# Kernel optimization log

Measured on AMD Instinct MI355X. Metric: run time of the kernel, lower is better.

Reference implementation:

```python
import jax, jax.numpy as jnp
import numpy as np

N_SP, N_SPAT = 20000, 10000
E_SS, E_BIP, E_SP = 160000, 320000, 320000
H, C = 4, 64  # GAT heads / per-head channels (hidden_channels=64, concat=False)
EPS = 1e-6


def _gat(xs, xd, row, col, ea, Ws, Wd, a_s, a_d, a_e, We, b, num_dst, heads, ch, self_loops, concat):
    # PyG GATConv with edge_dim: linear -> per-head additive attention -> softmax over incoming edges -> scatter-add
    hs = (xs @ Ws).reshape(-1, heads, ch)          # [Ns,H,C]
    hd = (xd @ Wd).reshape(-1, heads, ch)          # [Nd,H,C]
    al_s = jnp.sum(hs * a_s, -1)                   # [Ns,H]
    al_d = jnp.sum(hd * a_d, -1)                   # [Nd,H]
    if self_loops:
        # add_self_loops with fill_value='mean': loop edge_attr = mean of incoming edge_attr per node
        cnt = jax.ops.segment_sum(jnp.ones((row.shape[0],), ea.dtype), col, num_dst)
        loop_ea = jax.ops.segment_sum(ea, col, num_dst) / jnp.maximum(cnt, 1.0)[:, None]
        loops = jnp.arange(num_dst, dtype=row.dtype)
        row = jnp.concatenate([row, loops])
        col = jnp.concatenate([col, loops])
        ea = jnp.concatenate([ea, loop_ea], 0)
    he = (ea @ We).reshape(-1, heads, ch)          # [E,H,C]
    al = jax.nn.leaky_relu(al_s[row] + al_d[col] + jnp.sum(he * a_e, -1), 0.2)  # [E,H]
    m = jax.ops.segment_max(al, col, num_segments=num_dst)
    ex = jnp.exp(al - m[col])
    den = jax.ops.segment_sum(ex, col, num_segments=num_dst)
    alpha = ex / (den[col] + 1e-16)
    out = jax.ops.segment_sum(hs[row] * alpha[..., None], col, num_segments=num_dst)  # [Nd,H,C]
    out = out.reshape(num_dst, heads * ch) if concat else out.mean(1)
    return out + b


def setup_inputs() -> dict:
    key = jax.random.key(0)
    ks = iter(jax.random.split(key, 64))
    f = lambda shape: jax.random.normal(next(ks), shape, jnp.float32)
    w = lambda shape: f(shape) / np.sqrt(shape[0])
    inp = {}
    inp['species_x_mean'] = f((N_SP, 32))
    inp['species_x_std'] = jax.random.uniform(next(ks), (N_SP, 32), jnp.float32)
    inp['traits_nanmask'] = jax.random.bernoulli(next(ks), 0.4, (N_SP, 32))
    inp['species_x_gen'] = f((N_SP, 64))
    inp['species_x_phylo'] = f((N_SP, 128))
    inp['spatial_x'] = f((N_SPAT, 12))
    inp['spatial_global_data'] = f((N_SPAT, 4))
    ei = lambda e, ns, nd: jnp.stack([jax.random.randint(next(ks), (e,), 0, ns, jnp.int32),
                                      jax.random.randint(next(ks), (e,), 0, nd, jnp.int32)])
    inp['ss_edge_index'] = ei(E_SS, N_SPAT, N_SPAT)
    inp['ss_edge_attr'] = jax.random.uniform(next(ks), (E_SS, 1), jnp.float32)
    inp['bip_edge_index'] = ei(E_BIP, N_SPAT, N_SP)
    inp['bip_edge_attr'] = jax.random.uniform(next(ks), (E_BIP, 1), jnp.float32)
    inp['sp_edge_index'] = ei(E_SP, N_SP, N_SP)
    inp['sp_edge_attr'] = jax.random.uniform(next(ks), (E_SP, 1), jnp.float32)
    # GAT conv params: space_gnn (sg0, sg1), species_gnn (pg0, pg1)
    for nm, din in [('sg0', 16), ('sg1', 64), ('pg0', 128), ('pg1', 64)]:
        inp[nm + '_W'] = w((din, H * C))
        inp[nm + '_as'] = f((H, C)) * 0.1
        inp[nm + '_ad'] = f((H, C)) * 0.1
        inp[nm + '_ae'] = f((H, C)) * 0.1
        inp[nm + '_We'] = w((1, H * C))
        inp[nm + '_b'] = jnp.zeros((C,), jnp.float32)
    # bipartite GATConv: heads=1, concat=True, src dim=hidden=64, dst dim=in_gen+in_phylo=192
    inp['bp_Ws'] = w((64, 64))
    inp['bp_Wd'] = w((192, 64))
    inp['bp_as'] = f((1, 64)) * 0.1
    inp['bp_ad'] = f((1, 64)) * 0.1
    inp['bp_ae'] = f((1, 64)) * 0.1
    inp['bp_We'] = w((1, 64))
    inp['bp_b'] = jnp.zeros((64,), jnp.float32)
    inp['sl_W'] = w((288, 64))
    inp['sl_b'] = jnp.zeros((64,), jnp.float32)
    inp['fc_W'] = w((64, 64))
    inp['fc_b'] = jnp.zeros((64,), jnp.float32)
    return inp


def reference(species_x_mean, species_x_std, traits_nanmask, species_x_gen, species_x_phylo,
              spatial_x, spatial_global_data, ss_edge_index, ss_edge_attr, bip_edge_index,
              bip_edge_attr, sp_edge_index, sp_edge_attr,
              sg0_W, sg0_as, sg0_ad, sg0_ae, sg0_We, sg0_b,
              sg1_W, sg1_as, sg1_ad, sg1_ae, sg1_We, sg1_b,
              pg0_W, pg0_as, pg0_ad, pg0_ae, pg0_We, pg0_b,
              pg1_W, pg1_as, pg1_ad, pg1_ae, pg1_We, pg1_b,
              bp_Ws, bp_Wd, bp_as, bp_ad, bp_ae, bp_We, bp_b,
              sl_W, sl_b, fc_W, fc_b):
    # inference path: no trait masking -> visibility = observed mask
    vis = (~traits_nanmask).astype(jnp.float32)
    sp_in = jnp.concatenate([species_x_mean, species_x_std, vis, species_x_gen, species_x_phylo], 1)
    sp_in = jax.nn.relu(sp_in @ sl_W + sl_b)                      # [N_SP,64]
    # spatial GNN (2 GATConv layers, heads=4, concat=False, self loops)
    h = jnp.concatenate([spatial_x, spatial_global_data], 1)      # [N_SPAT,16]
    r, c = ss_edge_index[0], ss_edge_index[1]
    h = jax.nn.relu(_gat(h, h, r, c, ss_edge_attr, sg0_W, sg0_W, sg0_as, sg0_ad, sg0_ae, sg0_We, sg0_b, N_SPAT, H, C, True, False))
    h = jax.nn.relu(_gat(h, h, r, c, ss_edge_attr, sg1_W, sg1_W, sg1_as, sg1_ad, sg1_ae, sg1_We, sg1_b, N_SPAT, H, C, True, False))
    # bipartite spatial->species GATConv (heads=1, concat=True, no self loops)
    part = jnp.concatenate([species_x_gen, species_x_phylo], 1)   # [N_SP,192]
    br, bc = bip_edge_index[0], bip_edge_index[1]
    sts = jax.nn.relu(_gat(h, part, br, bc, bip_edge_attr, bp_Ws, bp_Wd, bp_as, bp_ad, bp_ae, bp_We, bp_b, N_SP, 1, 64, False, True))
    # species GNN (2 GATConv layers)
    x = jnp.concatenate([sts, sp_in], 1)                          # [N_SP,128]
    pr, pc = sp_edge_index[0], sp_edge_index[1]
    x = jax.nn.relu(_gat(x, x, pr, pc, sp_edge_attr, pg0_W, pg0_W, pg0_as, pg0_ad, pg0_ae, pg0_We, pg0_b, N_SP, H, C, True, False))
    x = jax.nn.relu(_gat(x, x, pr, pc, sp_edge_attr, pg1_W, pg1_W, pg1_as, pg1_ad, pg1_ae, pg1_We, pg1_b, N_SP, H, C, True, False))
    ms = x @ fc_W + fc_b                                          # [N_SP, 2*out]
    mean, log_std = jnp.split(ms, 2, axis=-1)
    std = jax.nn.softplus(log_std) + EPS
    return mean, std
```

## Files before the change

kernel.cpp:

```cpp
#include <hip/hip_runtime.h>
#include <hip/hip_bf16.h>

#define NSP   20000
#define NSPAT 10000
#define ESS   160000
#define EBIP  320000
#define ESP   320000

static inline int cdiv_host(long a, long b) { return (int)((a + b - 1) / b); }

__device__ __forceinline__ float wave_red_sum(float p) {
#pragma unroll
  for (int m = 32; m >= 1; m >>= 1) p += __shfl_xor(p, m, 64);
  return p;
}

__device__ __forceinline__ float bf2f(unsigned short u) {
  return __uint_as_float(((unsigned int)u) << 16);
}
__device__ __forceinline__ unsigned short f2bf(float f) {
  unsigned int u = __float_as_uint(f);
  unsigned int r = (u + 0x7FFF + ((u >> 16) & 1)) >> 16;
  return (unsigned short)r;
}

__global__ void build_pre_kernel(const float* __restrict__ mean, const float* __restrict__ stdv,
                                 const void* __restrict__ mask, const int* __restrict__ flag,
                                 const float* __restrict__ sx, const float* __restrict__ sg,
                                 float* __restrict__ spc96, float* __restrict__ h0) {
  const long totA = (long)NSP * 96;
  const long totB = (long)NSPAT * 16;
  int mode = *flag;
  for (long i = (long)blockIdx.x * blockDim.x + threadIdx.x; i < totA + totB;
       i += (long)gridDim.x * blockDim.x) {
    if (i < totA) {
      int n = (int)(i / 96), c = (int)(i % 96);
      float v;
      if (c < 32) v = mean[(long)n * 32 + c];
      else if (c < 64) v = stdv[(long)n * 32 + (c - 32)];
      else {
        long j = (long)n * 32 + (c - 64);
        int mv;
        if (mode == 0) mv = ((const int*)mask)[j];
        else if (mode == 2) mv = (((const float*)mask)[j] != 0.0f);
        else mv = (int)((const unsigned char*)mask)[j];
        v = mv ? 0.f : 1.f;
      }
      spc96[i] = v;
    } else {
      long k = i - totA;
      int n = (int)(k / 16), c = (int)(k % 16);
      h0[k] = (c < 12) ? sx[(long)n * 12 + c] : sg[(long)n * 4 + (c - 12)];
    }
  }
}

__global__ void count3_kernel(
    const int* c1, int E1, int* cp1, int* rnk1, int n1,
    const int* c2, int E2, int* cp2, int* rnk2, int n2,
    const int* c3, int E3, int* cp3, int* rnk3, int n3) {
  int total = E1 + E2 + E3;
  for (int i = blockIdx.x * blockDim.x + threadIdx.x; i < total; i += gridDim.x * blockDim.x) {
    int p = (i >> 8) & 7;
    if (i < E1) {
      int d = c1[i]; rnk1[i] = atomicAdd(&cp1[p * n1 + d], 1);
    } else if (i < E1 + E2) {
      int j = i - E1;
      int d = c2[j]; rnk2[j] = atomicAdd(&cp2[p * n2 + d], 1);
    } else {
      int j = i - E1 - E2;
      int d = c3[j]; rnk3[j] = atomicAdd(&cp3[p * n3 + d], 1);
    }
  }
}

__global__ void merge3_kernel(int* cp1, int* c1, int n1,
                              int* cp2, int* c2, int n2,
                              int* cp3, int* c3, int n3) {
  int i = blockIdx.x * blockDim.x + threadIdx.x;
  int total = n1 + n2 + n3;
  if (i >= total) return;
  int *cp, *c; int n, d;
  if (i < n1) { cp = cp1; c = c1; n = n1; d = i; }
  else if (i < n1 + n2) { cp = cp2; c = c2; n = n2; d = i - n1; }
  else { cp = cp3; c = c3; n = n3; d = i - n1 - n2; }
  int s = 0;
#pragma unroll
  for (int p = 0; p < 8; ++p) { int t = cp[p * n + d]; cp[p * n + d] = s; s += t; }
  c[d] = s;
}

__global__ __launch_bounds__(1024) void scan3_kernel(
    const int* cntA, int nA, int* ptrA,
    const int* cntB, int nB, int* ptrB,
    const int* cntC, int nC, int* ptrC) {
  const int* cnt; int n; int* ptr;
  if (blockIdx.x == 0) { cnt = cntA; n = nA; ptr = ptrA; }
  else if (blockIdx.x == 1) { cnt = cntB; n = nB; ptr = ptrB; }
  else { cnt = cntC; n = nC; ptr = ptrC; }
  __shared__ int part[1024];
  int t = threadIdx.x;
  int ch = (n + 1023) / 1024;
  int beg = t * ch, end = min(beg + ch, n);
  int s = 0;
  for (int i = beg; i < end; ++i) s += cnt[i];
  part[t] = s;
  __syncthreads();
  for (int off = 1; off < 1024; off <<= 1) {
    int v = (t >= off) ? part[t - off] : 0;
    __syncthreads();
    part[t] += v;
    __syncthreads();
  }
  int run = (t == 0) ? 0 : part[t - 1];
  for (int i = beg; i < end; ++i) { ptr[i] = run; run += cnt[i]; }
  if (t == 1023) ptr[n] = part[1023];
}

__global__ void scatter3_kernel(
    const int* r1, const int* c1, const float* e1, int E1, const int* p1, const int* cp1, const int* k1, int n1, int* s1, float* a1,
    const int* r2, const int* c2, const float* e2, int E2, const int* p2, const int* cp2, const int* k2, int n2, int* s2, float* a2,
    const int* r3, const int* c3, const float* e3, int E3, const int* p3, const int* cp3, const int* k3, int n3, int* s3, float* a3) {
  int total = E1 + E2 + E3;
  for (int i = blockIdx.x * blockDim.x + threadIdx.x; i < total; i += gridDim.x * blockDim.x) {
    int p = (i >> 8) & 7;
    if (i < E1) {
      int d = c1[i];
      int pos = p1[d] + cp1[p * n1 + d] + k1[i];
      s1[pos] = r1[i]; a1[pos] = e1[i];
    } else if (i < E1 + E2) {
      int j = i - E1;
      int d = c2[j];
      int pos = p2[d] + cp2[p * n2 + d] + k2[j];
      s2[pos] = r2[j]; a2[pos] = e2[j];
    } else {
      int j = i - E1 - E2;
      int d = c3[j];
      int pos = p3[d] + cp3[p * n3 + d] + k3[j];
      s3[pos] = r3[j]; a3[pos] = e3[j];
    }
  }
}

__global__ void leafin_csr2(const int* ptrA, const float* ceaA, int nA, float* leaA,
                            const int* ptrB, const float* ceaB, int nB, float* leaB) {
  int i = blockIdx.x * blockDim.x + threadIdx.x;
  if (i >= nA + nB) return;
  const int* ptr; const float* cea; float* lea; int d;
  if (i < nA) { ptr = ptrA; cea = ceaA; lea = leaA; d = i; }
  else { ptr = ptrB; cea = ceaB; lea = leaB; d = i - nA; }
  int e0 = ptr[d], e1 = ptr[d + 1];
  float s = 0.f;
  for (int e = e0; e < e1; ++e) s += cea[e];
  lea[d] = s / (float)max(e1 - e0, 1);
}

__global__ void dote_all_kernel(const float* __restrict__ We0, const float* __restrict__ ae0,
                                const float* __restrict__ We1, const float* __restrict__ ae1,
                                const float* __restrict__ Web, const float* __restrict__ aeb,
                                const float* __restrict__ We2, const float* __restrict__ ae2,
                                const float* __restrict__ We3, const float* __restrict__ ae3,
                                const unsigned int* __restrict__ mask,
                                float* __restrict__ dotes, int* __restrict__ flag) {
  int b = blockIdx.x, t = threadIdx.x;
  if (b == 5) {
    if (t < 64) {
      unsigned int w0 = mask[t], w1 = mask[t + 64], w2 = mask[t + 128], w3 = mask[t + 192];
      bool ai = (w0 <= 1u) && (w1 <= 1u) && (w2 <= 1u) && (w3 <= 1u);
      auto okf = [](unsigned int w) { return w == 0u || w == 0x3f800000u; };
      bool af = okf(w0) && okf(w1) && okf(w2) && okf(w3);
      unsigned long long bi = __ballot(ai), bf = __ballot(af);
      if (t == 0) *flag = (bi == ~0ull) ? 0 : ((bf == ~0ull) ? 2 : 1);
    }
    return;
  }
  const float *We, *ae;
  int n, off;
  switch (b) {
    case 0: We = We0; ae = ae0; n = 256; off = 0; break;
    case 1: We = We1; ae = ae1; n = 256; off = 4; break;
    case 2: We = Web; ae = aeb; n = 64;  off = 8; break;
    case 3: We = We2; ae = ae2; n = 256; off = 12; break;
    default: We = We3; ae = ae3; n = 256; off = 16; break;
  }
  if (t < n) {
    float p = wave_red_sum(We[t] * ae[t]);
    if ((t & 63) == 0) dotes[off + (t >> 6)] = p;
  }
}

struct XSrc { const float* p[5]; int w[5]; int n; };

__global__ __launch_bounds__(256) void proj64_kernel(
    XSrc xsrc, int M, int K,
    const float* __restrict__ W, const float* __restrict__ bias, int mode,
    const float* __restrict__ a_s, const float* __restrict__ a_d,
    float* __restrict__ al_s, float* __restrict__ al_d,
    float* __restrict__ Y, float* __restrict__ Y2) {
  constexpr int KC = 32;
  constexpr int BR = 32;
  constexpr int KCP = 36;
  __shared__ float wl[KC * 64];
  __shared__ float xl[BR * KCP];

  int t = threadIdx.x;
  int cg = t & 15, rg = t >> 4;
  int c0 = cg * 4;
  long row0 = (long)blockIdx.x * BR;

  float acc[2][4];
#pragma unroll
  for (int r = 0; r < 2; ++r)
#pragma unroll
    for (int j = 0; j < 4; ++j) acc[r][j] = 0.f;

  for (int k0 = 0; k0 < K; k0 += KC) {
    int seg = 0; int base = 0;
    while (k0 >= base + xsrc.w[seg]) { base += xsrc.w[seg]; ++seg; }
    const float* Xp = xsrc.p[seg];
    int stride = xsrc.w[seg];
    int kloc = k0 - base;

    __syncthreads();
    {
      const float4* ws = (const float4*)(W + (long)k0 * 64);
      float4* wd = (float4*)wl;
      wd[t] = ws[t];
      wd[t + 256] = ws[t + 256];
    }
    {
      int r = t >> 3, kq = (t & 7) * 4;
      long rr = row0 + r; if (rr >= M) rr = M - 1;
      float4 v = *(const float4*)(Xp + rr * stride + kloc + kq);
      *(float4*)(xl + r * KCP + kq) = v;
    }
    __syncthreads();

    for (int kg = 0; kg < KC; kg += 4) {
      float4 w0 = *(const float4*)(wl + (kg + 0) * 64 + c0);
      float4 w1 = *(const float4*)(wl + (kg + 1) * 64 + c0);
      float4 w2 = *(const float4*)(wl + (kg + 2) * 64 + c0);
      float4 w3 = *(const float4*)(wl + (kg + 3) * 64 + c0);
#pragma unroll
      for (int r = 0; r < 2; ++r) {
        float4 xv = *(const float4*)(xl + (rg * 2 + r) * KCP + kg);
        acc[r][0] = fmaf(xv.x, w0.x, acc[r][0]);
        acc[r][1] = fmaf(xv.x, w0.y, acc[r][1]);
        acc[r][2] = fmaf(xv.x, w0.z, acc[r][2]);
        acc[r][3] = fmaf(xv.x, w0.w, acc[r][3]);
        acc[r][0] = fmaf(xv.y, w1.x, acc[r][0]);
        acc[r][1] = fmaf(xv.y, w1.y, acc[r][1]);
        acc[r][2] = fmaf(xv.y, w1.z, acc[r][2]);
        acc[r][3] = fmaf(xv.y, w1.w, acc[r][3]);
        acc[r][0] = fmaf(xv.z, w2.x, acc[r][0]);
        acc[r][1] = fmaf(xv.z, w2.y, acc[r][1]);
        acc[r][2] = fmaf(xv.z, w2.z, acc[r][2]);
        acc[r][3] = fmaf(xv.z, w2.w, acc[r][3]);
        acc[r][0] = fmaf(xv.w, w3.x, acc[r][0]);
        acc[r][1] = fmaf(xv.w, w3.y, acc[r][1]);
        acc[r][2] = fmaf(xv.w, w3.z, acc[r][2]);
        acc[r][3] = fmaf(xv.w, w3.w, acc[r][3]);
      }
    }
  }

  float4 bv = make_float4(0.f, 0.f, 0.f, 0.f);
  float4 asv = make_float4(0.f, 0.f, 0.f, 0.f);
  float4 adv = make_float4(0.f, 0.f, 0.f, 0.f);
  if (bias) bv = *(const float4*)(bias + c0);
  if (a_s) asv = *(const float4*)(a_s + c0);
  if (a_d) adv = *(const float4*)(a_d + c0);

#pragma unroll
  for (int r = 0; r < 2; ++r) {
    long m = row0 + rg * 2 + r;
    bool ok = m < M;
    float v0 = acc[r][0] + bv.x, v1 = acc[r][1] + bv.y;
    float v2 = acc[r][2] + bv.z, v3 = acc[r][3] + bv.w;
    if (mode == 1) {
      if (ok)
        *(float4*)(Y + m * 64 + c0) = make_float4(
            fmaxf(v0, 0.f), fmaxf(v1, 0.f), fmaxf(v2, 0.f), fmaxf(v3, 0.f));
    } else if (mode == 2) {
      if (ok) {
        if (c0 < 32) {
          *(float4*)(Y + m * 32 + c0) = make_float4(v0, v1, v2, v3);
        } else {
          float4 o;
          o.x = fmaxf(v0, 0.f) + log1pf(__expf(-fabsf(v0))) + 1e-6f;
          o.y = fmaxf(v1, 0.f) + log1pf(__expf(-fabsf(v1))) + 1e-6f;
          o.z = fmaxf(v2, 0.f) + log1pf(__expf(-fabsf(v2))) + 1e-6f;
          o.w = fmaxf(v3, 0.f) + log1pf(__expf(-fabsf(v3))) + 1e-6f;
          *(float4*)(Y2 + m * 32 + (c0 - 32)) = o;
        }
      }
    } else if (ok && Y) {
      *(float4*)(Y + m * 64 + c0) = make_float4(v0, v1, v2, v3);
    }
    if (a_s) {
      float s = acc[r][0] * asv.x + acc[r][1] * asv.y + acc[r][2] * asv.z + acc[r][3] * asv.w;
      s += __shfl_xor(s, 1); s += __shfl_xor(s, 2);
      s += __shfl_xor(s, 4); s += __shfl_xor(s, 8);
      if (ok && cg == 0) al_s[m] = s;
    }
    if (a_d) {
      float s = acc[r][0] * adv.x + acc[r][1] * adv.y + acc[r][2] * adv.z + acc[r][3] * adv.w;
      s += __shfl_xor(s, 1); s += __shfl_xor(s, 2);
      s += __shfl_xor(s, 4); s += __shfl_xor(s, 8);
      if (ok && cg == 0) al_d[m] = s;
    }
  }
}

__global__ __launch_bounds__(256) void proj_kernel(
    XSrc xsrc, int M, int K,
    const float* __restrict__ W, const float* __restrict__ bias, int mode,
    const float* __restrict__ a_s, const float* __restrict__ a_d,
    float* __restrict__ al_s, float* __restrict__ al_d,
    float* __restrict__ Y, float* __restrict__ Y2) {
  constexpr int NOUT = 256;
  constexpr int KC = 32;
  constexpr int RPT = 8;
  constexpr int BR = 32;
  constexpr int KCP = 36;
  constexpr int H = 4;
  __shared__ float wl[KC * NOUT];
  __shared__ float xl[BR * KCP];

  int t = threadIdx.x;
  int cg = t & 63, rg = t >> 6;
  int c0 = cg * 4;
  long row0 = (long)blockIdx.x * BR;

  float acc[RPT][4];
#pragma unroll
  for (int r = 0; r < RPT; ++r)
#pragma unroll
    for (int j = 0; j < 4; ++j) acc[r][j] = 0.f;

  for (int k0 = 0; k0 < K; k0 += KC) {
    int kc = min(KC, K - k0);
    int seg = 0; int base = 0;
    while (k0 >= base + xsrc.w[seg]) { base += xsrc.w[seg]; ++seg; }
    const float* Xp = xsrc.p[seg];
    int stride = xsrc.w[seg];
    int kloc = k0 - base;

    __syncthreads();
    {
      const float4* wsrc = (const float4*)(W + (long)k0 * NOUT);
      float4* wdst = (float4*)wl;
      for (int i = t; i < (kc * NOUT) >> 2; i += 256) wdst[i] = wsrc[i];
    }
    for (int i = t; i < BR * 8; i += 256) {
      int r = i >> 3, kq = (i & 7) * 4;
      if (kq < kc) {
        long rr = row0 + r; if (rr >= M) rr = M - 1;
        float4 v = *(const float4*)(Xp + rr * stride + kloc + kq);
        *(float4*)(xl + r * KCP + kq) = v;
      }
    }
    __syncthreads();

    for (int kg = 0; kg < kc; kg += 4) {
      float4 w0 = *(const float4*)(wl + (kg + 0) * NOUT + c0);
      float4 w1 = *(const float4*)(wl + (kg + 1) * NOUT + c0);
      float4 w2 = *(const float4*)(wl + (kg + 2) * NOUT + c0);
      float4 w3 = *(const float4*)(wl + (kg + 3) * NOUT + c0);
      float4 xv[RPT];
#pragma unroll
      for (int r = 0; r < RPT; ++r)
        xv[r] = *(const float4*)(xl + (rg * RPT + r) * KCP + kg);
#pragma unroll
      for (int r = 0; r < RPT; ++r) {
        acc[r][0] = fmaf(xv[r].x, w0.x, acc[r][0]);
        acc[r][1] = fmaf(xv[r].x, w0.y, acc[r][1]);
        acc[r][2] = fmaf(xv[r].x, w0.z, acc[r][2]);
        acc[r][3] = fmaf(xv[r].x, w0.w, acc[r][3]);
        acc[r][0] = fmaf(xv[r].y, w1.x, acc[r][0]);
        acc[r][1] = fmaf(xv[r].y, w1.y, acc[r][1]);
        acc[r][2] = fmaf(xv[r].y, w1.z, acc[r][2]);
        acc[r][3] = fmaf(xv[r].y, w1.w, acc[r][3]);
        acc[r][0] = fmaf(xv[r].z, w2.x, acc[r][0]);
        acc[r][1] = fmaf(xv[r].z, w2.y, acc[r][1]);
        acc[r][2] = fmaf(xv[r].z, w2.z, acc[r][2]);
        acc[r][3] = fmaf(xv[r].z, w2.w, acc[r][3]);
        acc[r][0] = fmaf(xv[r].w, w3.x, acc[r][0]);
        acc[r][1] = fmaf(xv[r].w, w3.y, acc[r][1]);
        acc[r][2] = fmaf(xv[r].w, w3.z, acc[r][2]);
        acc[r][3] = fmaf(xv[r].w, w3.w, acc[r][3]);
      }
    }
  }

  float4 asv = make_float4(0.f, 0.f, 0.f, 0.f);
  float4 adv = make_float4(0.f, 0.f, 0.f, 0.f);
  if (a_s) asv = *(const float4*)(a_s + c0);
  if (a_d) adv = *(const float4*)(a_d + c0);

#pragma unroll
  for (int r = 0; r < RPT; ++r) {
    long m = row0 + (long)rg * RPT + r;
    bool ok = m < M;
    if (ok && mode == 3) {
      ushort4 o;
      o.x = f2bf(acc[r][0]); o.y = f2bf(acc[r][1]);
      o.z = f2bf(acc[r][2]); o.w = f2bf(acc[r][3]);
      *(ushort4*)((unsigned short*)Y + m * NOUT + c0) = o;
    }
    if (a_s) {
      float s = acc[r][0] * asv.x + acc[r][1] * asv.y + acc[r][2] * asv.z + acc[r][3] * asv.w;
      s += __shfl_xor(s, 1); s += __shfl_xor(s, 2);
      s += __shfl_xor(s, 4); s += __shfl_xor(s, 8);
      if (ok && (cg & 15) == 0) al_s[m * H + (c0 >> 6)] = s;
    }
    if (a_d) {
      float s = acc[r][0] * adv.x + acc[r][1] * adv.y + acc[r][2] * adv.z + acc[r][3] * adv.w;
      s += __shfl_xor(s, 1); s += __shfl_xor(s, 2);
      s += __shfl_xor(s, 4); s += __shfl_xor(s, 8);
      if (ok && (cg & 15) == 0) al_d[m * H + (c0 >> 6)] = s;
    }
  }
  (void)bias; (void)Y2;
}

__device__ __forceinline__ void fma4_bf(float4& a, float al, ushort4 u) {
  a.x = fmaf(al, bf2f(u.x), a.x); a.y = fmaf(al, bf2f(u.y), a.y);
  a.z = fmaf(al, bf2f(u.z), a.z); a.w = fmaf(al, bf2f(u.w), a.w);
}
__device__ __forceinline__ void scale4(float4& a, float s) {
  a.x *= s; a.y *= s; a.z *= s; a.w *= s;
}

template <bool SELFLOOP>
__global__ __launch_bounds__(256) void gat4_fused(
    int Nd, const int* __restrict__ dptr, const int* __restrict__ csr_src,
    const float* __restrict__ csr_ea, const float* __restrict__ al_s,
    const float* __restrict__ al_d, const float* __restrict__ dote,
    const float* __restrict__ loop_ea, const unsigned short* __restrict__ hs,
    const float* __restrict__ bias, float* __restrict__ out) {
  int wave = threadIdx.x >> 6, lane = threadIdx.x & 63;
  int n = blockIdx.x * 4 + wave;
  if (n >= Nd) return;
  int h = lane >> 4;
  float ald = al_d[(long)n * 4 + h];
  float de = dote[h];
  int e0 = dptr[n], e1 = dptr[n + 1];
  float m0 = -INFINITY, d0 = 0.f;
  float4 a0 = make_float4(0.f, 0.f, 0.f, 0.f);
  if (SELFLOOP) {
    float l = al_s[(long)n * 4 + h] + ald + loop_ea[n] * de;
    l = (l > 0.f) ? l : 0.2f * l;
    m0 = l; d0 = 1.f;
    ushort4 u = *(const ushort4*)(hs + (long)n * 256 + lane * 4);
    a0.x = bf2f(u.x); a0.y = bf2f(u.y); a0.z = bf2f(u.z); a0.w = bf2f(u.w);
  }
  float m1 = -INFINITY, d1 = 0.f;
  float4 a1 = make_float4(0.f, 0.f, 0.f, 0.f);
  int e = e0;
  for (; e + 2 <= e1; e += 2) {
    int s0 = csr_src[e], s1 = csr_src[e + 1];
    float l0 = al_s[(long)s0 * 4 + h] + ald + csr_ea[e] * de;
    float l1 = al_s[(long)s1 * 4 + h] + ald + csr_ea[e + 1] * de;
    l0 = (l0 > 0.f) ? l0 : 0.2f * l0;
    l1 = (l1 > 0.f) ? l1 : 0.2f * l1;
    ushort4 u0 = *(const ushort4*)(hs + (long)s0 * 256 + lane * 4);
    ushort4 u1 = *(const ushort4*)(hs + (long)s1 * 256 + lane * 4);
    if (l0 > m0) { float sc = __expf(m0 - l0); d0 *= sc; scale4(a0, sc); m0 = l0; }
    float ex0 = __expf(l0 - m0);
    d0 += ex0;
    fma4_bf(a0, ex0, u0);
    if (l1 > m1) { float sc = __expf(m1 - l1); d1 *= sc; scale4(a1, sc); m1 = l1; }
    float ex1 = __expf(l1 - m1);
    d1 += ex1;
    fma4_bf(a1, ex1, u1);
  }
  if (e < e1) {
    int s0 = csr_src[e];
    float l0 = al_s[(long)s0 * 4 + h] + ald + csr_ea[e] * de;
    l0 = (l0 > 0.f) ? l0 : 0.2f * l0;
    ushort4 u0 = *(const ushort4*)(hs + (long)s0 * 256 + lane * 4);
    if (l0 > m0) { float sc = __expf(m0 - l0); d0 *= sc; scale4(a0, sc); m0 = l0; }
    float ex0 = __expf(l0 - m0);
    d0 += ex0;
    fma4_bf(a0, ex0, u0);
  }
  if (m1 != -INFINITY) {
    float M = fmaxf(m0, m1);
    float sA = (m0 == -INFINITY) ? 0.f : __expf(m0 - M);
    float sB = __expf(m1 - M);
    d0 = d0 * sA + d1 * sB;
    a0.x = a0.x * sA + a1.x * sB; a0.y = a0.y * sA + a1.y * sB;
    a0.z = a0.z * sA + a1.z * sB; a0.w = a0.w * sA + a1.w * sB;
  }
  float inv = 1.f / (d0 + 1e-16f);
  scale4(a0, inv);
  a0.x += __shfl_xor(a0.x, 16); a0.y += __shfl_xor(a0.y, 16);
  a0.z += __shfl_xor(a0.z, 16); a0.w += __shfl_xor(a0.w, 16);
  a0.x += __shfl_xor(a0.x, 32); a0.y += __shfl_xor(a0.y, 32);
  a0.z += __shfl_xor(a0.z, 32); a0.w += __shfl_xor(a0.w, 32);
  if (lane < 16) {
    float4 b = *(const float4*)(bias + lane * 4);
    float4 o;
    o.x = fmaxf(a0.x * 0.25f + b.x, 0.f);
    o.y = fmaxf(a0.y * 0.25f + b.y, 0.f);
    o.z = fmaxf(a0.z * 0.25f + b.z, 0.f);
    o.w = fmaxf(a0.w * 0.25f + b.w, 0.f);
    *(float4*)(out + (long)n * 64 + lane * 4) = o;
  }
}

__global__ __launch_bounds__(256) void gat1_fused(
    int Nd, const int* __restrict__ dptr, const int* __restrict__ csr_src,
    const float* __restrict__ csr_ea, const float* __restrict__ al_s,
    const float* __restrict__ al_d, const float* __restrict__ dote,
    const float* __restrict__ hs, const float* __restrict__ bias,
    float* __restrict__ out) {
  int wave = threadIdx.x >> 6, lane = threadIdx.x & 63;
  int n = blockIdx.x * 4 + wave;
  if (n >= Nd) return;
  float ald = al_d[n];
  float de = dote[0];
  int e0 = dptr[n], e1 = dptr[n + 1];
  float m0 = -INFINITY, d0 = 0.f, acc0 = 0.f;
  float m1 = -INFINITY, d1 = 0.f, acc1 = 0.f;
  int e = e0;
  for (; e + 2 <= e1; e += 2) {
    int s0 = csr_src[e], s1 = csr_src[e + 1];
    float l0 = al_s[s0] + ald + csr_ea[e] * de;
    float l1 = al_s[s1] + ald + csr_ea[e + 1] * de;
    l0 = (l0 > 0.f) ? l0 : 0.2f * l0;
    l1 = (l1 > 0.f) ? l1 : 0.2f * l1;
    float h0 = hs[(long)s0 * 64 + lane];
    float h1 = hs[(long)s1 * 64 + lane];
    if (l0 > m0) { float sc = __expf(m0 - l0); d0 *= sc; acc0 *= sc; m0 = l0; }
    float ex0 = __expf(l0 - m0);
    d0 += ex0; acc0 = fmaf(ex0, h0, acc0);
    if (l1 > m1) { float sc = __expf(m1 - l1); d1 *= sc; acc1 *= sc; m1 = l1; }
    float ex1 = __expf(l1 - m1);
    d1 += ex1; acc1 = fmaf(ex1, h1, acc1);
  }
  if (e < e1) {
    int s0 = csr_src[e];
    float l0 = al_s[s0] + ald + csr_ea[e] * de;
    l0 = (l0 > 0.f) ? l0 : 0.2f * l0;
    float h0 = hs[(long)s0 * 64 + lane];
    if (l0 > m0) { float sc = __expf(m0 - l0); d0 *= sc; acc0 *= sc; m0 = l0; }
    float ex0 = __expf(l0 - m0);
    d0 += ex0; acc0 = fmaf(ex0, h0, acc0);
  }
  if (m1 != -INFINITY) {
    float M = fmaxf(m0, m1);
    float sA = (m0 == -INFINITY) ? 0.f : __expf(m0 - M);
    float sB = __expf(m1 - M);
    d0 = d0 * sA + d1 * sB;
    acc0 = acc0 * sA + acc1 * sB;
  }
  float o = acc0 / (d0 + 1e-16f);
  out[(long)n * 64 + lane] = fmaxf(o + bias[lane], 0.f);
}

extern "C" void kernel_launch(void* const* d_in, const int* in_sizes, int n_in,
                              void* d_out, int out_size, void* d_ws, size_t ws_size,
                              hipStream_t stream) {
  const float* sp_mean = (const float*)d_in[0];
  const float* sp_std  = (const float*)d_in[1];
  const void*  nanmask = d_in[2];
  const float* sp_gen  = (const float*)d_in[3];
  const float* sp_phy  = (const float*)d_in[4];
  const float* spat_x  = (const float*)d_in[5];
  const float* spat_g  = (const float*)d_in[6];
  const int*   ss_ei   = (const int*)d_in[7];
  const float* ss_ea   = (const float*)d_in[8];
  const int*   bip_ei  = (const int*)d_in[9];
  const float* bip_ea  = (const float*)d_in[10];
  const int*   sp_ei   = (const int*)d_in[11];
  const float* sp_ea   = (const float*)d_in[12];
  const float* sg0_W = (const float*)d_in[13]; const float* sg0_as = (const float*)d_in[14];
  const float* sg0_ad = (const float*)d_in[15]; const float* sg0_ae = (const float*)d_in[16];
  const float* sg0_We = (const float*)d_in[17]; const float* sg0_b = (const float*)d_in[18];
  const float* sg1_W = (const float*)d_in[19]; const float* sg1_as = (const float*)d_in[20];
  const float* sg1_ad = (const float*)d_in[21]; const float* sg1_ae = (const float*)d_in[22];
  const float* sg1_We = (const float*)d_in[23]; const float* sg1_b = (const float*)d_in[24];
  const float* pg0_W = (const float*)d_in[25]; const float* pg0_as = (const float*)d_in[26];
  const float* pg0_ad = (const float*)d_in[27]; const float* pg0_ae = (const float*)d_in[28];
  const float* pg0_We = (const float*)d_in[29]; const float* pg0_b = (const float*)d_in[30];
  const float* pg1_W = (const float*)d_in[31]; const float* pg1_as = (const float*)d_in[32];
  const float* pg1_ad = (const float*)d_in[33]; const float* pg1_ae = (const float*)d_in[34];
  const float* pg1_We = (const float*)d_in[35]; const float* pg1_b = (const float*)d_in[36];
  const float* bp_Ws = (const float*)d_in[37]; const float* bp_Wd = (const float*)d_in[38];
  const float* bp_as = (const float*)d_in[39]; const float* bp_ad = (const float*)d_in[40];
  const float* bp_ae = (const float*)d_in[41]; const float* bp_We = (const float*)d_in[42];
  const float* bp_b  = (const float*)d_in[43];
  const float* sl_W  = (const float*)d_in[44]; const float* sl_b  = (const float*)d_in[45];
  const float* fc_W  = (const float*)d_in[46]; const float* fc_b  = (const float*)d_in[47];

  char* wsb = (char*)d_ws;
  size_t off = 0;
  auto A = [&](size_t nbytes) -> void* {
    void* p = wsb + off;
    off += (nbytes + 255) & ~(size_t)255;
    return p;
  };
  int* ss_cp = (int*)A((size_t)8 * NSPAT * 4);
  int* bp_cp = (int*)A((size_t)8 * NSP * 4);
  int* pp_cp = (int*)A((size_t)8 * NSP * 4);
  size_t zbytes = off;
  int*   ss_cnt = (int*)A((NSPAT + 1) * 4);
  int*   bp_cnt = (int*)A((NSP + 1) * 4);
  int*   pp_cnt = (int*)A((NSP + 1) * 4);
  int*   flag  = (int*)A(4);
  float* dotes = (float*)A(5 * 4 * sizeof(float));
  float* alS   = (float*)A((size_t)NSP * 4 * 4);
  float* alD   = (float*)A((size_t)NSP * 4 * 4);
  float* spc96 = (float*)A((size_t)NSP * 96 * 4);
  float* sp_in = (float*)A((size_t)NSP * 64 * 4);
  float* h0    = (float*)A((size_t)NSPAT * 16 * 4);
  float* h_a   = (float*)A((size_t)NSPAT * 64 * 4);
  float* h_b   = (float*)A((size_t)NSPAT * 64 * 4);
  float* HS    = (float*)A((size_t)NSP * 256 * 4);
  float* sts   = (float*)A((size_t)NSP * 64 * 4);
  float* x1    = (float*)A((size_t)NSP * 64 * 4);
  int*   ss_ptr = (int*)A((NSPAT + 1) * 4);
  int*   ss_src = (int*)A((size_t)ESS * 4);
  float* ss_cea = (float*)A((size_t)ESS * 4);
  int*   ss_rnk = (int*)A((size_t)ESS * 4);
  float* ss_lea = (float*)A((size_t)NSPAT * 4);
  int*   bp_ptr = (int*)A((NSP + 1) * 4);
  int*   bp_src = (int*)A((size_t)EBIP * 4);
  float* bp_cea = (float*)A((size_t)EBIP * 4);
  int*   bp_rnk = (int*)A((size_t)EBIP * 4);
  int*   pp_ptr = (int*)A((NSP + 1) * 4);
  int*   pp_src = (int*)A((size_t)ESP * 4);
  float* pp_cea = (float*)A((size_t)ESP * 4);
  int*   pp_rnk = (int*)A((size_t)ESP * 4);
  float* pp_lea = (float*)A((size_t)NSP * 4);
  (void)ws_size; (void)in_sizes; (void)n_in; (void)out_size;

  const int TB = 256;
  hipMemsetAsync(wsb, 0, zbytes, stream);

  count3_kernel<<<cdiv_host(ESS + EBIP + ESP, TB), TB, 0, stream>>>(
      ss_ei + ESS, ESS, ss_cp, ss_rnk, NSPAT,
      bip_ei + EBIP, EBIP, bp_cp, bp_rnk, NSP,
      sp_ei + ESP, ESP, pp_cp, pp_rnk, NSP);
  merge3_kernel<<<cdiv_host(NSPAT + NSP + NSP, TB), TB, 0, stream>>>(
      ss_cp, ss_cnt, NSPAT, bp_cp, bp_cnt, NSP, pp_cp, pp_cnt, NSP);
  scan3_kernel<<<3, 1024, 0, stream>>>(ss_cnt, NSPAT, ss_ptr, bp_cnt, NSP, bp_ptr, pp_cnt, NSP, pp_ptr);
  scatter3_kernel<<<cdiv_host(ESS + EBIP + ESP, TB), TB, 0, stream>>>(
      ss_ei, ss_ei + ESS, ss_ea, ESS, ss_ptr, ss_cp, ss_rnk, NSPAT, ss_src, ss_cea,
      bip_ei, bip_ei + EBIP, bip_ea, EBIP, bp_ptr, bp_cp, bp_rnk, NSP, bp_src, bp_cea,
      sp_ei, sp_ei + ESP, sp_ea, ESP, pp_ptr, pp_cp, pp_rnk, NSP, pp_src, pp_cea);
  leafin_csr2<<<cdiv_host(NSPAT + NSP, TB), TB, 0, stream>>>(
      ss_ptr, ss_cea, NSPAT, ss_lea, pp_ptr, pp_cea, NSP, pp_lea);

  dote_all_kernel<<<6, 256, 0, stream>>>(sg0_We, sg0_ae, sg1_We, sg1_ae, bp_We, bp_ae,
                                         pg0_We, pg0_ae, pg1_We, pg1_ae,
                                         (const unsigned int*)nanmask, dotes, flag);

  build_pre_kernel<<<cdiv_host((long)NSP * 96 + (long)NSPAT * 16, TB), TB, 0, stream>>>(
      sp_mean, sp_std, nanmask, flag, spat_x, spat_g, spc96, h0);

  {
    XSrc xs{}; xs.p[0] = spc96; xs.w[0] = 96; xs.p[1] = sp_gen; xs.w[1] = 64;
    xs.p[2] = sp_phy; xs.w[2] = 128; xs.n = 3;
    proj64_kernel<<<cdiv_host(NSP, 32), TB, 0, stream>>>(xs, NSP, 288, sl_W, sl_b, 1,
        nullptr, nullptr, nullptr, nullptr, sp_in, nullptr);
  }

  {
    XSrc xs{}; xs.p[0] = h0; xs.w[0] = 16; xs.n = 1;
    proj_kernel<<<cdiv_host(NSPAT, 32), TB, 0, stream>>>(xs, NSPAT, 16, sg0_W, nullptr, 3,
        sg0_as, sg0_ad, alS, alD, HS, nullptr);
  }
  gat4_fused<true><<<cdiv_host(NSPAT, 4), TB, 0, stream>>>(
      NSPAT, ss_ptr, ss_src, ss_cea, alS, alD, dotes + 0, ss_lea,
      (const unsigned short*)HS, sg0_b, h_a);
  {
    XSrc xs{}; xs.p[0] = h_a; xs.w[0] = 64; xs.n = 1;
    proj_kernel<<<cdiv_host(NSPAT, 32), TB, 0, stream>>>(xs, NSPAT, 64, sg1_W, nullptr, 3,
        sg1_as, sg1_ad, alS, alD, HS, nullptr);
  }
  gat4_fused<true><<<cdiv_host(NSPAT, 4), TB, 0, stream>>>(
      NSPAT, ss_ptr, ss_src, ss_cea, alS, alD, dotes + 4, ss_lea,
      (const unsigned short*)HS, sg1_b, h_b);

  {
    XSrc xs{}; xs.p[0] = h_b; xs.w[0] = 64; xs.n = 1;
    proj64_kernel<<<cdiv_host(NSPAT, 32), TB, 0, stream>>>(xs, NSPAT, 64, bp_Ws, nullptr, 0,
        bp_as, nullptr, alS, nullptr, h_a, nullptr);
  }
  {
    XSrc xs{}; xs.p[0] = sp_gen; xs.w[0] = 64; xs.p[1] = sp_phy; xs.w[1] = 128; xs.n = 2;
    proj64_kernel<<<cdiv_host(NSP, 32), TB, 0, stream>>>(xs, NSP, 192, bp_Wd, nullptr, 0,
        nullptr, bp_ad, nullptr, alD, nullptr, nullptr);
  }
  gat1_fused<<<cdiv_host(NSP, 4), TB, 0, stream>>>(
      NSP, bp_ptr, bp_src, bp_cea, alS, alD, dotes + 8, h_a, bp_b, sts);

  {
    XSrc xs{}; xs.p[0] = sts; xs.w[0] = 64; xs.p[1] = sp_in; xs.w[1] = 64; xs.n = 2;
    proj_kernel<<<cdiv_host(NSP, 32), TB, 0, stream>>>(xs, NSP, 128, pg0_W, nullptr, 3,
        pg0_as, pg0_ad, alS, alD, HS, nullptr);
  }
  gat4_fused<true><<<cdiv_host(NSP, 4), TB, 0, stream>>>(
      NSP, pp_ptr, pp_src, pp_cea, alS, alD, dotes + 12, pp_lea,
      (const unsigned short*)HS, pg0_b, x1);
  {
    XSrc xs{}; xs.p[0] = x1; xs.w[0] = 64; xs.n = 1;
    proj_kernel<<<cdiv_host(NSP, 32), TB, 0, stream>>>(xs, NSP, 64, pg1_W, nullptr, 3,
        pg1_as, pg1_ad, alS, alD, HS, nullptr);
  }
  gat4_fused<true><<<cdiv_host(NSP, 4), TB, 0, stream>>>(
      NSP, pp_ptr, pp_src, pp_cea, alS, alD, dotes + 16, pp_lea,
      (const unsigned short*)HS, pg1_b, sts);

  {
    XSrc xs{}; xs.p[0] = sts; xs.w[0] = 64; xs.n = 1;
    proj64_kernel<<<cdiv_host(NSP, 32), TB, 0, stream>>>(xs, NSP, 64, fc_W, fc_b, 2,
        nullptr, nullptr, nullptr, nullptr, (float*)d_out, (float*)d_out + (long)NSP * 32);
  }
}
```

Measured before the change: 524.9 us.

## Merge small preprocessing and projection kernels to cut launch count

Moves the nan-mask flag detection into an extra block of the edge-count kernel. Merges the leaf-mean, edge-dot and input-build kernels into one launch split by block range. Batches the bipartite destination projection with the species-input projection in a dual-job launch, using separate alpha buffers so it can run early. This removes several launches and serialisation points, at the cost of a larger parameter struct. There is a possible ordering risk: misc_kernel reads the flag written by count3, which is safe only because launches on one stream run in order.

New measurement: 498.3 us. -5.1%, faster.

```diff
diff --git a/kernel.cpp b/kernel.cpp
--- a/kernel.cpp
+++ b/kernel.cpp
@@ -24,53 +24,35 @@
   return (unsigned short)r;
 }
 
-__global__ void build_pre_kernel(const float* __restrict__ mean, const float* __restrict__ stdv,
-                                 const void* __restrict__ mask, const int* __restrict__ flag,
-                                 const float* __restrict__ sx, const float* __restrict__ sg,
-                                 float* __restrict__ spc96, float* __restrict__ h0) {
-  const long totA = (long)NSP * 96;
-  const long totB = (long)NSPAT * 16;
-  int mode = *flag;
-  for (long i = (long)blockIdx.x * blockDim.x + threadIdx.x; i < totA + totB;
-       i += (long)gridDim.x * blockDim.x) {
-    if (i < totA) {
-      int n = (int)(i / 96), c = (int)(i % 96);
-      float v;
-      if (c < 32) v = mean[(long)n * 32 + c];
-      else if (c < 64) v = stdv[(long)n * 32 + (c - 32)];
-      else {
-        long j = (long)n * 32 + (c - 64);
-        int mv;
-        if (mode == 0) mv = ((const int*)mask)[j];
-        else if (mode == 2) mv = (((const float*)mask)[j] != 0.0f);
-        else mv = (int)((const unsigned char*)mask)[j];
-        v = mv ? 0.f : 1.f;
-      }
-      spc96[i] = v;
-    } else {
-      long k = i - totA;
-      int n = (int)(k / 16), c = (int)(k % 16);
-      h0[k] = (c < 12) ? sx[(long)n * 12 + c] : sg[(long)n * 4 + (c - 12)];
-    }
-  }
-}
-
 __global__ void count3_kernel(
     const int* c1, int E1, int* cp1, int* rnk1, int n1,
     const int* c2, int E2, int* cp2, int* rnk2, int n2,
-    const int* c3, int E3, int* cp3, int* rnk3, int n3) {
+    const int* c3, int E3, int* cp3, int* rnk3, int n3,
+    const unsigned int* __restrict__ mask, int* __restrict__ flag) {
+  int b = blockIdx.x, t = threadIdx.x;
+  if (b == gridDim.x - 1) {
+    if (t < 64) {
+      unsigned int w0 = mask[t], w1 = mask[t + 64], w2 = mask[t + 128], w3 = mask[t + 192];
+      bool ai = (w0 <= 1u) && (w1 <= 1u) && (w2 <= 1u) && (w3 <= 1u);
+      auto okf = [](unsigned int w) { return w == 0u || w == 0x3f800000u; };
+      bool af = okf(w0) && okf(w1) && okf(w2) && okf(w3);
+      unsigned long long bi = __ballot(ai), bf = __ballot(af);
+      if (t == 0) *flag = (bi == ~0ull) ? 0 : ((bf == ~0ull) ? 2 : 1);
+    }
+    return;
+  }
+  int i = b * 256 + t;
   int total = E1 + E2 + E3;
-  for (int i = blockIdx.x * blockDim.x + threadIdx.x; i < total; i += gridDim.x * blockDim.x) {
-    int p = (i >> 8) & 7;
-    if (i < E1) {
-      int d = c1[i]; rnk1[i] = atomicAdd(&cp1[p * n1 + d], 1);
-    } else if (i < E1 + E2) {
-      int j = i - E1;
-      int d = c2[j]; rnk2[j] = atomicAdd(&cp2[p * n2 + d], 1);
-    } else {
-      int j = i - E1 - E2;
-      int d = c3[j]; rnk3[j] = atomicAdd(&cp3[p * n3 + d], 1);
-    }
+  if (i >= total) return;
+  int p = (i >> 8) & 7;
+  if (i < E1) {
+    int d = c1[i]; rnk1[i] = atomicAdd(&cp1[p * n1 + d], 1);
+  } else if (i < E1 + E2) {
+    int j = i - E1;
+    int d = c2[j]; rnk2[j] = atomicAdd(&cp2[p * n2 + d], 1);
+  } else {
+    int j = i - E1 - E2;
+    int d = c3[j]; rnk3[j] = atomicAdd(&cp3[p * n3 + d], 1);
   }
 }
 
@@ -142,71 +124,91 @@
   }
 }
 
-__global__ void leafin_csr2(const int* ptrA, const float* ceaA, int nA, float* leaA,
-                            const int* ptrB, const float* ceaB, int nB, float* leaB) {
-  int i = blockIdx.x * blockDim.x + threadIdx.x;
-  if (i >= nA + nB) return;
-  const int* ptr; const float* cea; float* lea; int d;
-  if (i < nA) { ptr = ptrA; cea = ceaA; lea = leaA; d = i; }
-  else { ptr = ptrB; cea = ceaB; lea = leaB; d = i - nA; }
-  int e0 = ptr[d], e1 = ptr[d + 1];
-  float s = 0.f;
-  for (int e = e0; e < e1; ++e) s += cea[e];
-  lea[d] = s / (float)max(e1 - e0, 1);
-}
-
-__global__ void dote_all_kernel(const float* __restrict__ We0, const float* __restrict__ ae0,
-                                const float* __restrict__ We1, const float* __restrict__ ae1,
-                                const float* __restrict__ Web, const float* __restrict__ aeb,
-                                const float* __restrict__ We2, const float* __restrict__ ae2,
-                                const float* __restrict__ We3, const float* __restrict__ ae3,
-                                const unsigned int* __restrict__ mask,
-                                float* __restrict__ dotes, int* __restrict__ flag) {
+__global__ void misc_kernel(
+    const int* __restrict__ ss_ptr, const float* __restrict__ ss_cea, float* __restrict__ ss_lea,
+    const int* __restrict__ pp_ptr, const float* __restrict__ pp_cea, float* __restrict__ pp_lea,
+    const float* __restrict__ We0, const float* __restrict__ ae0,
+    const float* __restrict__ We1, const float* __restrict__ ae1,
+    const float* __restrict__ Web, const float* __restrict__ aeb,
+    const float* __restrict__ We2, const float* __restrict__ ae2,
+    const float* __restrict__ We3, const float* __restrict__ ae3,
+    float* __restrict__ dotes,
+    const float* __restrict__ mean, const float* __restrict__ stdv,
+    const void* __restrict__ mask, const int* __restrict__ flag,
+    const float* __restrict__ sx, const float* __restrict__ sg,
+    float* __restrict__ spc96, float* __restrict__ h0) {
   int b = blockIdx.x, t = threadIdx.x;
-  if (b == 5) {
-    if (t < 64) {
-      unsigned int w0 = mask[t], w1 = mask[t + 64], w2 = mask[t + 128], w3 = mask[t + 192];
-      bool ai = (w0 <= 1u) && (w1 <= 1u) && (w2 <= 1u) && (w3 <= 1u);
-      auto okf = [](unsigned int w) { return w == 0u || w == 0x3f800000u; };
-      bool af = okf(w0) && okf(w1) && okf(w2) && okf(w3);
-      unsigned long long bi = __ballot(ai), bf = __ballot(af);
-      if (t == 0) *flag = (bi == ~0ull) ? 0 : ((bf == ~0ull) ? 2 : 1);
-    }
-    return;
-  }
-  const float *We, *ae;
-  int n, off;
-  switch (b) {
-    case 0: We = We0; ae = ae0; n = 256; off = 0; break;
-    case 1: We = We1; ae = ae1; n = 256; off = 4; break;
-    case 2: We = Web; ae = aeb; n = 64;  off = 8; break;
-    case 3: We = We2; ae = ae2; n = 256; off = 12; break;
-    default: We = We3; ae = ae3; n = 256; off = 16; break;
-  }
-  if (t < n) {
-    float p = wave_red_sum(We[t] * ae[t]);
-    if ((t & 63) == 0) dotes[off + (t >> 6)] = p;
+  if (b < 118) {
+    int i = b * 256 + t;
+    if (i >= NSPAT + NSP) return;
+    const int* ptr; const float* cea; float* lea; int d;
+    if (i < NSPAT) { ptr = ss_ptr; cea = ss_cea; lea = ss_lea; d = i; }
+    else { ptr = pp_ptr; cea = pp_cea; lea = pp_lea; d = i - NSPAT; }
+    int e0 = ptr[d], e1 = ptr[d + 1];
+    float s = 0.f;
+    for (int e = e0; e < e1; ++e) s += cea[e];
+    lea[d] = s / (float)max(e1 - e0, 1);
+  } else if (b < 123) {
+    int lb = b - 118;
+    const float *We, *ae; int n, off;
+    switch (lb) {
+      case 0: We = We0; ae = ae0; n = 256; off = 0; break;
+      case 1: We = We1; ae = ae1; n = 256; off = 4; break;
+      case 2: We = Web; ae = aeb; n = 64;  off = 8; break;
+      case 3: We = We2; ae = ae2; n = 256; off = 12; break;
+      default: We = We3; ae = ae3; n = 256; off = 16; break;
+    }
+    if (t < n) {
+      float p = wave_red_sum(We[t] * ae[t]);
+      if ((t & 63) == 0) dotes[off + (t >> 6)] = p;
+    }
+  } else {
+    const long totA = (long)NSP * 96;
+    const long totB = (long)NSPAT * 16;
+    long i = (long)(b - 123) * 256 + t;
+    if (i >= totA + totB) return;
+    int mode = *flag;
+    if (i < totA) {
+      int n = (int)(i / 96), c = (int)(i % 96);
+      float v;
+      if (c < 32) v = mean[(long)n * 32 + c];
+      else if (c < 64) v = stdv[(long)n * 32 + (c - 32)];
+      else {
+        long j = (long)n * 32 + (c - 64);
+        int mv;
+        if (mode == 0) mv = ((const int*)mask)[j];
+        else if (mode == 2) mv = (((const float*)mask)[j] != 0.0f);
+        else mv = (int)((const unsigned char*)mask)[j];
+        v = mv ? 0.f : 1.f;
+      }
+      spc96[i] = v;
+    } else {
+      long k = i - totA;
+      int n = (int)(k / 16), c = (int)(k % 16);
+      h0[k] = (c < 12) ? sx[(long)n * 12 + c] : sg[(long)n * 4 + (c - 12)];
+    }
   }
 }
 
 struct XSrc { const float* p[5]; int w[5]; int n; };
-
-__global__ __launch_bounds__(256) void proj64_kernel(
-    XSrc xsrc, int M, int K,
-    const float* __restrict__ W, const float* __restrict__ bias, int mode,
-    const float* __restrict__ a_s, const float* __restrict__ a_d,
-    float* __restrict__ al_s, float* __restrict__ al_d,
-    float* __restrict__ Y, float* __restrict__ Y2) {
+struct PJob {
+  XSrc xs; int M, K;
+  const float* W; const float* bias; int mode;
+  const float* a_s; const float* a_d;
+  float* al_s; float* al_d;
+  float* Y; float* Y2;
+};
+
+__device__ __forceinline__ void proj64_body(const PJob& J, int bid,
+                                            float* wl, float* xl) {
   constexpr int KC = 32;
   constexpr int BR = 32;
   constexpr int KCP = 36;
-  __shared__ float wl[KC * 64];
-  __shared__ float xl[BR * KCP];
-
   int t = threadIdx.x;
+  long row0 = (long)bid * BR;
+  if (row0 >= J.M) return;
   int cg = t & 15, rg = t >> 4;
   int c0 = cg * 4;
-  long row0 = (long)blockIdx.x * BR;
 
   float acc[2][4];
 #pragma unroll
@@ -214,23 +216,23 @@
 #pragma unroll
     for (int j = 0; j < 4; ++j) acc[r][j] = 0.f;
 
-  for (int k0 = 0; k0 < K; k0 += KC) {
+  for (int k0 = 0; k0 < J.K; k0 += KC) {
     int seg = 0; int base = 0;
-    while (k0 >= base + xsrc.w[seg]) { base += xsrc.w[seg]; ++seg; }
-    const float* Xp = xsrc.p[seg];
-    int stride = xsrc.w[seg];
+    while (k0 >= base + J.xs.w[seg]) { base += J.xs.w[seg]; ++seg; }
+    const float* Xp = J.xs.p[seg];
+    int stride = J.xs.w[seg];
     int kloc = k0 - base;
 
     __syncthreads();
     {
-      const float4* ws = (const float4*)(W + (long)k0 * 64);
+      const float4* ws = (const float4*)(J.W + (long)k0 * 64);
       float4* wd = (float4*)wl;
       wd[t] = ws[t];
       wd[t + 256] = ws[t + 256];
     }
     {
       int r = t >> 3, kq = (t & 7) * 4;
-      long rr = row0 + r; if (rr >= M) rr = M - 1;
+      long rr = row0 + r; if (rr >= J.M) rr = J.M - 1;
       float4 v = *(const float4*)(Xp + rr * stride + kloc + kq);
       *(float4*)(xl + r * KCP + kq) = v;
     }
@@ -267,49 +269,56 @@
   float4 bv = make_float4(0.f, 0.f, 0.f, 0.f);
   float4 asv = make_float4(0.f, 0.f, 0.f, 0.f);
   float4 adv = make_float4(0.f, 0.f, 0.f, 0.f);
-  if (bias) bv = *(const float4*)(bias + c0);
-  if (a_s) asv = *(const float4*)(a_s + c0);
-  if (a_d) adv = *(const float4*)(a_d + c0);
+  if (J.bias) bv = *(const float4*)(J.bias + c0);
+  if (J.a_s) asv = *(const float4*)(J.a_s + c0);
+  if (J.a_d) adv = *(const float4*)(J.a_d + c0);
 
 #pragma unroll
   for (int r = 0; r < 2; ++r) {
     long m = row0 + rg * 2 + r;
-    bool ok = m < M;
+    bool ok = m < J.M;
     float v0 = acc[r][0] + bv.x, v1 = acc[r][1] + bv.y;
     float v2 = acc[r][2] + bv.z, v3 = acc[r][3] + bv.w;
-    if (mode == 1) {
+    if (J.mode == 1) {
       if (ok)
-        *(float4*)(Y + m * 64 + c0) = make_float4(
+        *(float4*)(J.Y + m * 64 + c0) = make_float4(
             fmaxf(v0, 0.f), fmaxf(v1, 0.f), fmaxf(v2, 0.f), fmaxf(v3, 0.f));
-    } else if (mode == 2) {
+    } else if (J.mode == 2) {
       if (ok) {
         if (c0 < 32) {
-          *(float4*)(Y + m * 32 + c0) = make_float4(v0, v1, v2, v3);
+          *(float4*)(J.Y + m * 32 + c0) = make_float4(v0, v1, v2, v3);
         } else {
           float4 o;
           o.x = fmaxf(v0, 0.f) + log1pf(__expf(-fabsf(v0))) + 1e-6f;
           o.y = fmaxf(v1, 0.f) + log1pf(__expf(-fabsf(v1))) + 1e-6f;
           o.z = fmaxf(v2, 0.f) + log1pf(__expf(-fabsf(v2))) + 1e-6f;
           o.w = fmaxf(v3, 0.f) + log1pf(__expf(-fabsf(v3))) + 1e-6f;
-          *(float4*)(Y2 + m * 32 + (c0 - 32)) = o;
+          *(float4*)(J.Y2 + m * 32 + (c0 - 32)) = o;
         }
       }
-    } else if (ok && Y) {
-      *(float4*)(Y + m * 64 + c0) = make_float4(v0, v1, v2, v3);
-    }
-    if (a_s) {
+    } else if (ok && J.Y) {
+      *(float4*)(J.Y + m * 64 + c0) = make_float4(v0, v1, v2, v3);
+    }
+    if (J.a_s) {
       float s = acc[r][0] * asv.x + acc[r][1] * asv.y + acc[r][2] * asv.z + acc[r][3] * asv.w;
       s += __shfl_xor(s, 1); s += __shfl_xor(s, 2);
       s += __shfl_xor(s, 4); s += __shfl_xor(s, 8);
-      if (ok && cg == 0) al_s[m] = s;
-    }
-    if (a_d) {
+      if (ok && cg == 0) J.al_s[m] = s;
+    }
+    if (J.a_d) {
       float s = acc[r][0] * adv.x + acc[r][1] * adv.y + acc[r][2] * adv.z + acc[r][3] * adv.w;
       s += __shfl_xor(s, 1); s += __shfl_xor(s, 2);
       s += __shfl_xor(s, 4); s += __shfl_xor(s, 8);
-      if (ok && cg == 0) al_d[m] = s;
-    }
-  }
+      if (ok && cg == 0) J.al_d[m] = s;
+    }
+  }
+}
+
+__global__ __launch_bounds__(256) void proj64x2_kernel(PJob j0, PJob j1, int nb0) {
+  __shared__ float wl[32 * 64];
+  __shared__ float xl[32 * 36];
+  if ((int)blockIdx.x < nb0) proj64_body(j0, blockIdx.x, wl, xl);
+  else proj64_body(j1, blockIdx.x - nb0, wl, xl);
 }
 
 __global__ __launch_bounds__(256) void proj_kernel(
@@ -613,6 +622,8 @@
   float* dotes = (float*)A(5 * 4 * sizeof(float));
   float* alS   = (float*)A((size_t)NSP * 4 * 4);
   float* alD   = (float*)A((size_t)NSP * 4 * 4);
+  float* alSb  = (float*)A((size_t)NSPAT * 4);
+  float* alDb  = (float*)A((size_t)NSP * 4);
   float* spc96 = (float*)A((size_t)NSP * 96 * 4);
   float* sp_in = (float*)A((size_t)NSP * 64 * 4);
   float* h0    = (float*)A((size_t)NSPAT * 16 * 4);
@@ -640,10 +651,11 @@
   const int TB = 256;
   hipMemsetAsync(wsb, 0, zbytes, stream);
 
-  count3_kernel<<<cdiv_host(ESS + EBIP + ESP, TB), TB, 0, stream>>>(
+  count3_kernel<<<cdiv_host(ESS + EBIP + ESP, TB) + 1, TB, 0, stream>>>(
       ss_ei + ESS, ESS, ss_cp, ss_rnk, NSPAT,
       bip_ei + EBIP, EBIP, bp_cp, bp_rnk, NSP,
-      sp_ei + ESP, ESP, pp_cp, pp_rnk, NSP);
+      sp_ei + ESP, ESP, pp_cp, pp_rnk, NSP,
+      (const unsigned int*)nanmask, flag);
   merge3_kernel<<<cdiv_host(NSPAT + NSP + NSP, TB), TB, 0, stream>>>(
       ss_cp, ss_cnt, NSPAT, bp_cp, bp_cnt, NSP, pp_cp, pp_cnt, NSP);
   scan3_kernel<<<3, 1024, 0, stream>>>(ss_cnt, NSPAT, ss_ptr, bp_cnt, NSP, bp_ptr, pp_cnt, NSP, pp_ptr);
@@ -651,21 +663,21 @@
       ss_ei, ss_ei + ESS, ss_ea, ESS, ss_ptr, ss_cp, ss_rnk, NSPAT, ss_src, ss_cea,
       bip_ei, bip_ei + EBIP, bip_ea, EBIP, bp_ptr, bp_cp, bp_rnk, NSP, bp_src, bp_cea,
       sp_ei, sp_ei + ESP, sp_ea, ESP, pp_ptr, pp_cp, pp_rnk, NSP, pp_src, pp_cea);
-  leafin_csr2<<<cdiv_host(NSPAT + NSP, TB), TB, 0, stream>>>(
-      ss_ptr, ss_cea, NSPAT, ss_lea, pp_ptr, pp_cea, NSP, pp_lea);
-
-  dote_all_kernel<<<6, 256, 0, stream>>>(sg0_We, sg0_ae, sg1_We, sg1_ae, bp_We, bp_ae,
-                                         pg0_We, pg0_ae, pg1_We, pg1_ae,
-                                         (const unsigned int*)nanmask, dotes, flag);
-
-  build_pre_kernel<<<cdiv_host((long)NSP * 96 + (long)NSPAT * 16, TB), TB, 0, stream>>>(
-      sp_mean, sp_std, nanmask, flag, spat_x, spat_g, spc96, h0);
+
+  misc_kernel<<<123 + cdiv_host((long)NSP * 96 + (long)NSPAT * 16, TB), TB, 0, stream>>>(
+      ss_ptr, ss_cea, ss_lea, pp_ptr, pp_cea, pp_lea,
+      sg0_We, sg0_ae, sg1_We, sg1_ae, bp_We, bp_ae, pg0_We, pg0_ae, pg1_We, pg1_ae,
+      dotes, sp_mean, sp_std, nanmask, flag, spat_x, spat_g, spc96, h0);
 
   {
-    XSrc xs{}; xs.p[0] = spc96; xs.w[0] = 96; xs.p[1] = sp_gen; xs.w[1] = 64;
-    xs.p[2] = sp_phy; xs.w[2] = 128; xs.n = 3;
-    proj64_kernel<<<cdiv_host(NSP, 32), TB, 0, stream>>>(xs, NSP, 288, sl_W, sl_b, 1,
-        nullptr, nullptr, nullptr, nullptr, sp_in, nullptr);
+    PJob j0{}; j0.xs.p[0] = spc96; j0.xs.w[0] = 96; j0.xs.p[1] = sp_gen; j0.xs.w[1] = 64;
+    j0.xs.p[2] = sp_phy; j0.xs.w[2] = 128; j0.xs.n = 3;
+    j0.M = NSP; j0.K = 288; j0.W = sl_W; j0.bias = sl_b; j0.mode = 1; j0.Y = sp_in;
+    PJob j1{}; j1.xs.p[0] = sp_gen; j1.xs.w[0] = 64; j1.xs.p[1] = sp_phy; j1.xs.w[1] = 128;
+    j1.xs.n = 2;
+    j1.M = NSP; j1.K = 192; j1.W = bp_Wd; j1.mode = 0; j1.a_d = bp_ad; j1.al_d = alDb;
+    int nb0 = cdiv_host(NSP, 32);
+    proj64x2_kernel<<<nb0 + cdiv_host(NSP, 32), TB, 0, stream>>>(j0, j1, nb0);
   }
 
   {
@@ -686,17 +698,14 @@
       (const unsigned short*)HS, sg1_b, h_b);
 
   {
-    XSrc xs{}; xs.p[0] = h_b; xs.w[0] = 64; xs.n = 1;
-    proj64_kernel<<<cdiv_host(NSPAT, 32), TB, 0, stream>>>(xs, NSPAT, 64, bp_Ws, nullptr, 0,
-        bp_as, nullptr, alS, nullptr, h_a, nullptr);
-  }
-  {
-    XSrc xs{}; xs.p[0] = sp_gen; xs.w[0] = 64; xs.p[1] = sp_phy; xs.w[1] = 128; xs.n = 2;
-    proj64_kernel<<<cdiv_host(NSP, 32), TB, 0, stream>>>(xs, NSP, 192, bp_Wd, nullptr, 0,
-        nullptr, bp_ad, nullptr, alD, nullptr, nullptr);
+    PJob j0{}; j0.xs.p[0] = h_b; j0.xs.w[0] = 64; j0.xs.n = 1;
+    j0.M = NSPAT; j0.K = 64; j0.W = bp_Ws; j0.mode = 0;
+    j0.a_s = bp_as; j0.al_s = alSb; j0.Y = h_a;
+    int nb0 = cdiv_host(NSPAT, 32);
+    proj64x2_kernel<<<nb0, TB, 0, stream>>>(j0, j0, nb0);
   }
   gat1_fused<<<cdiv_host(NSP, 4), TB, 0, stream>>>(
-      NSP, bp_ptr, bp_src, bp_cea, alS, alD, dotes + 8, h_a, bp_b, sts);
+      NSP, bp_ptr, bp_src, bp_cea, alSb, alDb, dotes + 8, h_a, bp_b, sts);
 
   {
     XSrc xs{}; xs.p[0] = sts; xs.w[0] = 64; xs.p[1] = sp_in; xs.w[1] = 64; xs.n = 2;
@@ -716,8 +725,10 @@
       (const unsigned short*)HS, pg1_b, sts);
 
   {
-    XSrc xs{}; xs.p[0] = sts; xs.w[0] = 64; xs.n = 1;
-    proj64_kernel<<<cdiv_host(NSP, 32), TB, 0, stream>>>(xs, NSP, 64, fc_W, fc_b, 2,
-        nullptr, nullptr, nullptr, nullptr, (float*)d_out, (float*)d_out + (long)NSP * 32);
-  }
-}
+    PJob j0{}; j0.xs.p[0] = sts; j0.xs.w[0] = 64; j0.xs.n = 1;
+    j0.M = NSP; j0.K = 64; j0.W = fc_W; j0.bias = fc_b; j0.mode = 2;
+    j0.Y = (float*)d_out; j0.Y2 = (float*)d_out + (long)NSP * 32;
+    int nb0 = cdiv_host(NSP, 32);
+    proj64x2_kernel<<<nb0, TB, 0, stream>>>(j0, j0, nb0);
+  }
+}
```
